# Performance work log

Hardware: AMD Instinct MI355X
Metric: run time of the kernel (lower is better)

## Reference

```python
import jax, jax.numpy as jnp
import numpy as np

N_NODES = 100000
N_EDGES = 1600000
IN_FEATS = 256
HIDDEN = 128
N_CLASSES = 128
NEG_SLOPE = 0.2


def setup_inputs() -> dict:
    key = jax.random.key(0)
    ks = jax.random.split(key, 12)
    inp = {
        "features": jax.random.normal(ks[0], (N_NODES, IN_FEATS), dtype=jnp.float32),
        "src": jax.random.randint(ks[1], (N_EDGES,), 0, N_NODES, dtype=jnp.int32),
        "dst": jax.random.randint(ks[2], (N_EDGES,), 0, N_NODES, dtype=jnp.int32),
        # layer 1 params (Xavier-ish scale)
        "W1": jax.random.normal(ks[3], (HIDDEN, IN_FEATS), dtype=jnp.float32) / np.sqrt(IN_FEATS),
        "al1": jax.random.normal(ks[4], (HIDDEN,), dtype=jnp.float32) / np.sqrt(HIDDEN),
        "ar1": jax.random.normal(ks[5], (HIDDEN,), dtype=jnp.float32) / np.sqrt(HIDDEN),
        "b1": jnp.zeros((HIDDEN,), dtype=jnp.float32),
        # layer 2 params
        "W2": jax.random.normal(ks[6], (N_CLASSES, HIDDEN), dtype=jnp.float32) / np.sqrt(HIDDEN),
        "al2": jax.random.normal(ks[7], (N_CLASSES,), dtype=jnp.float32) / np.sqrt(N_CLASSES),
        "ar2": jax.random.normal(ks[8], (N_CLASSES,), dtype=jnp.float32) / np.sqrt(N_CLASSES),
        "b2": jnp.zeros((N_CLASSES,), dtype=jnp.float32),
    }
    return inp


def _gat_conv(x, W, attn_l, attn_r, bias, src, dst):
    """Single-head DGL GATConv: fc -> edge leaky-relu scores -> segment softmax over dst -> scatter-sum."""
    h = x @ W.T                                   # [N, D]
    el = h @ attn_l                               # [N]
    er = h @ attn_r                               # [N]
    e = jax.nn.leaky_relu(el[src] + er[dst], NEG_SLOPE)   # [E]
    # numerically stable segment softmax over incoming edges of each dst node
    m = jax.ops.segment_max(e, dst, num_segments=N_NODES)          # [N] (-inf for empty)
    ex = jnp.exp(e - m[dst])                                       # [E]
    s = jax.ops.segment_sum(ex, dst, num_segments=N_NODES)         # [N]
    alpha = ex / s[dst]                                            # [E]
    out = jax.ops.segment_sum(h[src] * alpha[:, None], dst, num_segments=N_NODES)
    return out + bias


def reference(features, src, dst, W1, al1, ar1, b1, W2, al2, ar2, b2):
    x = _gat_conv(features, W1, al1, ar1, b1, src, dst)
    x = jax.nn.elu(x)
    return _gat_conv(x, W2, al2, ar2, b2, src, dst)
```

## Files before the change

### kernel.cpp

```cpp
#include <hip/hip_runtime.h>

typedef unsigned short u16;
typedef unsigned int u32;

#define NEG_SLOPE 0.2f
#define BSHIFT 8
#define MAXBUCK 1024

using short8 = __attribute__((ext_vector_type(8))) short;
using float4v = __attribute__((ext_vector_type(4))) float;

__device__ __forceinline__ float bfu(u16 v) { return __uint_as_float(((u32)v) << 16); }
__device__ __forceinline__ float bflo(u32 u) { return __uint_as_float(u << 16); }
__device__ __forceinline__ float bfhi(u32 u) { return __uint_as_float(u & 0xffff0000u); }
__device__ __forceinline__ u16 f2bf(float f) {
  u32 x = __float_as_uint(f);
  return (u16)((x + 0x7fffu + ((x >> 16) & 1u)) >> 16);
}
__device__ __forceinline__ float loadf(const void* p, int idx, int isbf) {
  return isbf ? bfu(((const u16*)p)[idx]) : ((const float*)p)[idx];
}

__global__ __launch_bounds__(256) void detect_dtype(const u32* __restrict__ w,
                                                    int nwords, int* __restrict__ flag) {
  __shared__ int cnt;
  if (threadIdx.x == 0) cnt = 0;
  __syncthreads();
  int c = 0;
  for (int i = threadIdx.x; i < nwords; i += 256) {
    u32 e = (w[i] >> 7) & 0xFFu;
    c += (e >= 0x60u && e <= 0x90u) ? 1 : 0;
  }
  atomicAdd(&cnt, c);
  __syncthreads();
  if (threadIdx.x == 0) flag[0] = (cnt * 2 > nwords) ? 1 : 0;
}

__global__ __launch_bounds__(256) void scanA(int* __restrict__ a,
                                             int* __restrict__ bsum, int M) {
  __shared__ int sh[256];
  int t = threadIdx.x;
  int idx = blockIdx.x * 256 + t;
  int v = (idx < M) ? a[idx] : 0;
  sh[t] = v;
  __syncthreads();
  for (int off = 1; off < 256; off <<= 1) {
    int y = (t >= off) ? sh[t - off] : 0;
    __syncthreads();
    sh[t] += y;
    __syncthreads();
  }
  if (idx < M) a[idx] = sh[t] - v;
  if (t == 255) bsum[blockIdx.x] = sh[255];
}

__global__ __launch_bounds__(512) void scanBseq(int* __restrict__ a, int MB) {
  __shared__ int sh[512];
  __shared__ int carry;
  int t = threadIdx.x;
  if (t == 0) carry = 0;
  __syncthreads();
  for (int base = 0; base < MB; base += 512) {
    int v = (base + t < MB) ? a[base + t] : 0;
    sh[t] = v;
    __syncthreads();
    for (int off = 1; off < 512; off <<= 1) {
      int y = (t >= off) ? sh[t - off] : 0;
      __syncthreads();
      sh[t] += y;
      __syncthreads();
    }
    int c0 = carry;
    int excl = sh[t] - v + c0;
    int tot = sh[511];
    __syncthreads();
    if (t == 0) carry = c0 + tot;
    if (base + t < MB) a[base + t] = excl;
    __syncthreads();
  }
}

__global__ __launch_bounds__(256) void scanC(int* __restrict__ a,
                                             const int* __restrict__ boff, int M) {
  int idx = blockIdx.x * 256 + threadIdx.x;
  if (idx < M) a[idx] += boff[blockIdx.x];
}

__global__ __launch_bounds__(256) void part_scatter(const int* __restrict__ src,
                                                    const int* __restrict__ dst,
                                                    const int* __restrict__ Gh,
                                                    int* __restrict__ pd,
                                                    int* __restrict__ ps,
                                                    int E, int PB, int nbuck) {
  __shared__ int cur[MAXBUCK];
  int t = threadIdx.x;
  int blk = blockIdx.x;
  for (int i = t; i < nbuck; i += 256) cur[i] = Gh[(size_t)i * PB + blk];
  __syncthreads();
  int pbase = blk * 4096;
#pragma unroll
  for (int j = 0; j < 16; ++j) {
    int e = pbase + j * 256 + t;
    if (e < E) {
      int d = dst[e];
      int s = src[e];
      u32 b = (u32)d >> BSHIFT;
      if (b < (u32)nbuck) {
        int slot = atomicAdd(&cur[b], 1);
        if ((u32)slot < (u32)E) {
          pd[slot] = d;
          ps[slot] = s;
        }
      }
    }
  }
}

__global__ __launch_bounds__(256) void bucket_sort(const int* __restrict__ pd,
                                                   const int* __restrict__ ps,
                                                   const int* __restrict__ Gh,
                                                   int* __restrict__ indptr,
                                                   int* __restrict__ ssrc,
                                                   int E, int N, int PB, int nbuck) {
  __shared__ int bins[256];
  __shared__ int sh[256];
  __shared__ int cur[256];
  int t = threadIdx.x;
  int b = blockIdx.x;
  int base = Gh[(size_t)b * PB];
  int nextb = (b + 1 < nbuck) ? Gh[(size_t)(b + 1) * PB] : E;
  int sz = nextb - base;

  bins[t] = 0;
  __syncthreads();
  for (int i = t; i < sz; i += 256) atomicAdd(&bins[pd[base + i] & 255], 1);
  __syncthreads();

  int v = bins[t];
  sh[t] = v;
  __syncthreads();
  for (int off = 1; off < 256; off <<= 1) {
    int y = (t >= off) ? sh[t - off] : 0;
    __syncthreads();
    sh[t] += y;
    __syncthreads();
  }
  int excl = sh[t] - v;
  int node = b * 256 + t;
  if (node < N) indptr[node] = base + excl;
  if (b == 0 && t == 0) indptr[N] = E;
  cur[t] = excl;
  __syncthreads();

  for (int i = t; i < sz; i += 256) {
    int d = pd[base + i];
    int slot = atomicAdd(&cur[d & 255], 1);
    u32 gidx = (u32)(base + slot);
    if (gidx < (u32)E) ssrc[gidx] = ps[base + i];
  }
}

__global__ __launch_bounds__(256) void bsw_build(const void* __restrict__ W,
                                                 u16* __restrict__ Bsw, int K,
                                                 const int* __restrict__ dflag) {
  const int isbf = dflag[0];
  int t = blockIdx.x * 256 + threadIdx.x;
  int total = (K / 32) * 8 * 64;
  if (t >= total) return;
  int lane = t & 63;
  int c = (t >> 6) & 7;
  int ktile = t >> 9;
  int n = lane & 15, q = lane >> 4;
  int col = c * 16 + n;
  u16 vals[8];
#pragma unroll
  for (int j = 0; j < 8; ++j) {
    int k = ktile * 32 + q * 8 + j;
    int idx = col * K + k;
    vals[j] = isbf ? ((const u16*)W)[idx] : f2bf(((const float*)W)[idx]);
  }
  *(uint4*)(Bsw + (size_t)t * 8) = *(uint4*)vals;
}

template <int K, int ISBF>
__device__ __forceinline__ void gemm_core(const void* __restrict__ Xv,
                                          const u16* __restrict__ Bsw,
                                          const int* mclamp, int q, int lane,
                                          float4v acc[2][8]) {
  constexpr int NT = K / 32;
  const uint4* btb = (const uint4*)Bsw + lane;
  if (ISBF) {
    const u16* X0 = (const u16*)Xv + (size_t)mclamp[0] * K + q * 8;
    const u16* X1 = (const u16*)Xv + (size_t)mclamp[1] * K + q * 8;
    short8 a0 = *(const short8*)X0;
    short8 a1 = *(const short8*)X1;
#pragma unroll
    for (int t = 0; t < NT; ++t) {
      short8 n0 = a0, n1 = a1;
      if (t + 1 < NT) {
        n0 = *(const short8*)(X0 + (t + 1) * 32);
        n1 = *(const short8*)(X1 + (t + 1) * 32);
      }
      const uint4* bt = btb + (size_t)t * 8 * 64;
#pragma unroll
      for (int c = 0; c < 8; ++c) {
        uint4 bw = bt[c * 64];
        short8 bf = *(short8*)&bw;
        acc[0][c] = __builtin_amdgcn_mfma_f32_16x16x32_bf16(a0, bf, acc[0][c], 0, 0, 0);
        acc[1][c] = __builtin_amdgcn_mfma_f32_16x16x32_bf16(a1, bf, acc[1][c], 0, 0, 0);
      }
      a0 = n0;
      a1 = n1;
    }
  } else {
    const float* X0 = (const float*)Xv + (size_t)mclamp[0] * K + q * 8;
    const float* X1 = (const float*)Xv + (size_t)mclamp[1] * K + q * 8;
    float4 f00 = *(const float4*)X0, f01 = *(const float4*)(X0 + 4);
    float4 f10 = *(const float4*)X1, f11 = *(const float4*)(X1 + 4);
#pragma unroll
    for (int t = 0; t < NT; ++t) {
      float4 g00 = f00, g01 = f01, g10 = f10, g11 = f11;
      if (t + 1 < NT) {
        g00 = *(const float4*)(X0 + (t + 1) * 32);
        g01 = *(const float4*)(X0 + (t + 1) * 32 + 4);
        g10 = *(const float4*)(X1 + (t + 1) * 32);
        g11 = *(const float4*)(X1 + (t + 1) * 32 + 4);
      }
      u16 t0[8] = {f2bf(f00.x), f2bf(f00.y), f2bf(f00.z), f2bf(f00.w),
                   f2bf(f01.x), f2bf(f01.y), f2bf(f01.z), f2bf(f01.w)};
      u16 t1[8] = {f2bf(f10.x), f2bf(f10.y), f2bf(f10.z), f2bf(f10.w),
                   f2bf(f11.x), f2bf(f11.y), f2bf(f11.z), f2bf(f11.w)};
      short8 a0 = *(short8*)t0;
      short8 a1 = *(short8*)t1;
      const uint4* bt = btb + (size_t)t * 8 * 64;
#pragma unroll
      for (int c = 0; c < 8; ++c) {
        uint4 bw = bt[c * 64];
        short8 bf = *(short8*)&bw;
        acc[0][c] = __builtin_amdgcn_mfma_f32_16x16x32_bf16(a0, bf, acc[0][c], 0, 0, 0);
        acc[1][c] = __builtin_amdgcn_mfma_f32_16x16x32_bf16(a1, bf, acc[1][c], 0, 0, 0);
      }
      f00 = g00; f01 = g01; f10 = g10; f11 = g11;
    }
  }
}

template <int K, int DYNA>
__device__ __forceinline__ void gemm_body(int bix, const void* __restrict__ Xv,
                                          const u16* __restrict__ Bsw,
                                          u16* __restrict__ Hb,
                                          const void* __restrict__ al,
                                          const void* __restrict__ ar,
                                          float* __restrict__ el_,
                                          float* __restrict__ er_, int N,
                                          const int* __restrict__ dflag) {
  const int isbfP = dflag[0];
  int tid = threadIdx.x;
  int w = tid >> 6, lane = tid & 63;
  int n = lane & 15, q = lane >> 4;
  int base = bix * 128 + w * 32;

  int mclamp[2];
#pragma unroll
  for (int mt = 0; mt < 2; ++mt) {
    int m = base + mt * 16 + n;
    mclamp[mt] = (m < N) ? m : 0;
  }

  float alv[8], arv[8];
#pragma unroll
  for (int c = 0; c < 8; ++c) {
    alv[c] = loadf(al, c * 16 + n, isbfP);
    arv[c] = loadf(ar, c * 16 + n, isbfP);
  }

  float4v acc[2][8];
#pragma unroll
  for (int mt = 0; mt < 2; ++mt)
#pragma unroll
    for (int c = 0; c < 8; ++c) acc[mt][c] = (float4v){0.f, 0.f, 0.f, 0.f};

  if (DYNA == 0 || isbfP) {
    gemm_core<K, 1>(Xv, Bsw, mclamp, q, lane, acc);
  } else {
    gemm_core<K, 0>(Xv, Bsw, mclamp, q, lane, acc);
  }

#pragma unroll
  for (int mt = 0; mt < 2; ++mt)
#pragma unroll
    for (int c = 0; c < 8; ++c) {
#pragma unroll
      for (int r = 0; r < 4; ++r) {
        int row = base + mt * 16 + q * 4 + r;
        if (row < N) Hb[(size_t)row * 128 + c * 16 + n] = f2bf(acc[mt][c][r]);
      }
    }

#pragma unroll
  for (int mt = 0; mt < 2; ++mt)
#pragma unroll
    for (int r = 0; r < 4; ++r) {
      float sl = 0.f, sr = 0.f;
#pragma unroll
      for (int c = 0; c < 8; ++c) {
        float v = acc[mt][c][r];
        sl = fmaf(v, alv[c], sl);
        sr = fmaf(v, arv[c], sr);
      }
#pragma unroll
      for (int off = 1; off < 16; off <<= 1) {
        sl += __shfl_xor(sl, off);
        sr += __shfl_xor(sr, off);
      }
      if (n == 0) {
        int row = base + mt * 16 + q * 4 + r;
        if (row < N) {
          el_[row] = sl;
          er_[row] = sr;
        }
      }
    }
}

template <int K, int DYNA>
__global__ __launch_bounds__(256) void gemm_mfma(const void* __restrict__ Xv,
                                                 const u16* __restrict__ Bsw,
                                                 u16* __restrict__ Hb,
                                                 const void* __restrict__ al,
                                                 const void* __restrict__ ar,
                                                 float* __restrict__ el_,
                                                 float* __restrict__ er_, int N,
                                                 const int* __restrict__ dflag) {
  gemm_body<K, DYNA>(blockIdx.x, Xv, Bsw, Hb, al, ar, el_, er_, N, dflag);
}

template <int K, int DYNA>
__global__ __launch_bounds__(256) void fused_gemm_hist(
    const void* __restrict__ Xv, const u16* __restrict__ Bsw, u16* __restrict__ Hb,
    const void* __restrict__ al, const void* __restrict__ ar,
    float* __restrict__ el_, float* __restrict__ er_, int N,
    const int* __restrict__ dflag, int gemm_blocks,
    const int* __restrict__ dst, int* __restrict__ Gh, int E, int PB, int nbuck) {
  __shared__ int hcnt[MAXBUCK];
  int bix = (int)blockIdx.x;
  if (bix < gemm_blocks) {
    gemm_body<K, DYNA>(bix, Xv, Bsw, Hb, al, ar, el_, er_, N, dflag);
    return;
  }
  int pblk = bix - gemm_blocks;
  int t = threadIdx.x;
  for (int i = t; i < nbuck; i += 256) hcnt[i] = 0;
  __syncthreads();
  int pbase = pblk * 4096;
#pragma unroll
  for (int j = 0; j < 16; ++j) {
    int e = pbase + j * 256 + t;
    if (e < E) {
      u32 b = (u32)dst[e] >> BSHIFT;
      if (b < (u32)nbuck) atomicAdd(&hcnt[b], 1);
    }
  }
  __syncthreads();
  for (int i = t; i < nbuck; i += 256) Gh[(size_t)i * PB + pblk] = hcnt[i];
}

template <int MODE>
__global__ __launch_bounds__(256) void agg_kernel(const u32* __restrict__ Hb,
                                                  const float* __restrict__ el,
                                                  const float* __restrict__ er,
                                                  const int* __restrict__ indptr,
                                                  const int* __restrict__ ssrc,
                                                  const void* __restrict__ bias,
                                                  void* __restrict__ outv, int N,
                                                  const int* __restrict__ dflag) {
  const int isbf = dflag[0];
  int tid = threadIdx.x;
  int n = blockIdx.x * 4 + (tid >> 6);
  int lane = tid & 63;
  if (n >= N) return;

  int beg = indptr[n];
  int end = indptr[n + 1];
  float ern = er[n];

  float aa0 = 0.f, aa1 = 0.f;
  float m_run = -INFINITY, l_run = 0.f;

  for (int p = beg; p < end; p += 64) {
    int rem = end - p;
    int valid = lane < rem;
    int ide = valid ? ssrc[p + lane] : 0;

    float sc = el[ide] + ern;
    sc = (sc > 0.f) ? sc : NEG_SLOPE * sc;
    sc = valid ? sc : -INFINITY;

    float mc = sc;
#pragma unroll
    for (int off = 1; off < 64; off <<= 1) mc = fmaxf(mc, __shfl_xor(mc, off));

    float m_new = fmaxf(m_run, mc);
    float corr = __expf(m_run - m_new);
    float pe = __expf(sc - m_new);

    float ls = pe;
#pragma unroll
    for (int off = 1; off < 64; off <<= 1) ls += __shfl_xor(ls, off);

    l_run = l_run * corr + ls;
    aa0 *= corr;
    aa1 *= corr;
    m_run = m_new;

    int cl = (rem < 64) ? rem : 64;
    int e = 0;
    for (; e + 8 <= cl; e += 8) {
      int id_[8];
      u32 h_[8];
#pragma unroll
      for (int k = 0; k < 8; ++k) id_[k] = __builtin_amdgcn_readlane(ide, e + k);
#pragma unroll
      for (int k = 0; k < 8; ++k) h_[k] = Hb[(size_t)id_[k] * 64 + lane];
#pragma unroll
      for (int k = 0; k < 8; ++k) {
        float pk = __int_as_float(__builtin_amdgcn_readlane(__float_as_int(pe), e + k));
        aa0 = fmaf(pk, bflo(h_[k]), aa0);
        aa1 = fmaf(pk, bfhi(h_[k]), aa1);
      }
    }
    for (; e + 4 <= cl; e += 4) {
      int id_[4];
      u32 h_[4];
#pragma unroll
      for (int k = 0; k < 4; ++k) id_[k] = __builtin_amdgcn_readlane(ide, e + k);
#pragma unroll
      for (int k = 0; k < 4; ++k) h_[k] = Hb[(size_t)id_[k] * 64 + lane];
#pragma unroll
      for (int k = 0; k < 4; ++k) {
        float pk = __int_as_float(__builtin_amdgcn_readlane(__float_as_int(pe), e + k));
        aa0 = fmaf(pk, bflo(h_[k]), aa0);
        aa1 = fmaf(pk, bfhi(h_[k]), aa1);
      }
    }
    for (; e < cl; ++e) {
      int i0 = __builtin_amdgcn_readlane(ide, e);
      u32 h0 = Hb[(size_t)i0 * 64 + lane];
      float p0 = __int_as_float(__builtin_amdgcn_readlane(__float_as_int(pe), e));
      aa0 = fmaf(p0, bflo(h0), aa0);
      aa1 = fmaf(p0, bfhi(h0), aa1);
    }
  }

  float inv = (l_run > 0.f) ? 1.f / l_run : 0.f;
  float o0 = aa0 * inv + loadf(bias, 2 * lane, isbf);
  float o1 = aa1 * inv + loadf(bias, 2 * lane + 1, isbf);

  if (MODE == 0) {
    o0 = (o0 > 0.f) ? o0 : (__expf(o0) - 1.f);
    o1 = (o1 > 0.f) ? o1 : (__expf(o1) - 1.f);
    ((u32*)outv)[(size_t)n * 64 + lane] = (u32)f2bf(o0) | ((u32)f2bf(o1) << 16);
  } else {
    if (isbf) {
      ((u32*)outv)[(size_t)n * 64 + lane] = (u32)f2bf(o0) | ((u32)f2bf(o1) << 16);
    } else {
      ((float2*)outv)[(size_t)n * 64 + lane] = make_float2(o0, o1);
    }
  }
}


extern "C" void kernel_launch(void* const* d_in, const int* in_sizes, int n_in,
                              void* d_out, int out_size, void* d_ws, size_t ws_size,
                              hipStream_t stream) {
  const int IN_FEATS = 256, HID = 128;
  const void* features = d_in[0];
  const int* src = (const int*)d_in[1];
  const int* dst = (const int*)d_in[2];
  const void* W1 = d_in[3];
  const void* al1 = d_in[4];
  const void* ar1 = d_in[5];
  const void* b1 = d_in[6];
  const void* W2 = d_in[7];
  const void* al2 = d_in[8];
  const void* ar2 = d_in[9];
  const void* b2 = d_in[10];

  const int N = in_sizes[0] / IN_FEATS;
  const int E = in_sizes[1];

  char* p = (char*)d_ws;
  auto alloc = [&](size_t bytes) -> void* {
    void* q = (void*)p;
    p += (bytes + 255) & ~(size_t)255;
    return q;
  };
  int* dflag = (int*)alloc(256);
  u16* Bsw1 = (u16*)alloc((size_t)(IN_FEATS / 32) * 8 * 64 * 8 * 2);
  u16* Bsw2 = (u16*)alloc((size_t)(HID / 32) * 8 * 64 * 8 * 2);
  u16* hb = (u16*)alloc((size_t)N * HID * 2);
  u16* x = (u16*)alloc((size_t)N * HID * 2);
  float* el = (float*)alloc((size_t)N * 4);
  float* er = (float*)alloc((size_t)N * 4);
  int* indptr = (int*)alloc((size_t)(N + 1) * 4);

  const int nbuck = (N + 255) >> BSHIFT;
  const int PB = (E + 4095) / 4096;
  const int M = nbuck * PB;
  const int MB1 = (M + 255) / 256;

  int* Gh = (int*)alloc((size_t)M * 4);
  int* bsumA = (int*)alloc((size_t)MB1 * 4);
  int* ssrc = (int*)alloc((size_t)E * 4);

  int* pd = (int*)x;
  int* ps = (int*)((char*)x + (((size_t)E * 4 + 255) & ~(size_t)255));

  const int GEMM_B = (N + 127) / 128;
  const int NODE_B = (N + 3) / 4;

  detect_dtype<<<1, 256, 0, stream>>>((const u32*)features, 4096, dflag);
  bsw_build<<<((IN_FEATS / 32) * 8 * 64 + 255) / 256, 256, 0, stream>>>(W1, Bsw1, IN_FEATS, dflag);
  bsw_build<<<((HID / 32) * 8 * 64 + 255) / 256, 256, 0, stream>>>(W2, Bsw2, HID, dflag);

  fused_gemm_hist<IN_FEATS, 1><<<GEMM_B + PB, 256, 0, stream>>>(
      features, Bsw1, hb, al1, ar1, el, er, N, dflag, GEMM_B, dst, Gh, E, PB, nbuck);

  scanA<<<MB1, 256, 0, stream>>>(Gh, bsumA, M);
  scanBseq<<<1, 512, 0, stream>>>(bsumA, MB1);
  scanC<<<MB1, 256, 0, stream>>>(Gh, bsumA, M);

  part_scatter<<<PB, 256, 0, stream>>>(src, dst, Gh, pd, ps, E, PB, nbuck);
  bucket_sort<<<nbuck, 256, 0, stream>>>(pd, ps, Gh, indptr, ssrc, E, N, PB, nbuck);

  agg_kernel<0><<<NODE_B, 256, 0, stream>>>((const u32*)hb, el, er, indptr, ssrc, b1, (void*)x, N, dflag);

  gemm_mfma<HID, 0><<<GEMM_B, 256, 0, stream>>>((const void*)x, Bsw2, hb, al2, ar2, el, er, N, dflag);
  agg_kernel<1><<<NODE_B, 256, 0, stream>>>((const u32*)hb, el, er, indptr, ssrc, b2, d_out, N, dflag);
}
```

Baseline: 468.7 us.

## Fold scan offsets into consumers, stage GEMM weights in LDS, specialize low-degree aggregation

```diff
diff --git a/kernel.cpp b/kernel.cpp
--- a/kernel.cpp
+++ b/kernel.cpp
@@ -9,6 +9,7 @@
 
 using short8 = __attribute__((ext_vector_type(8))) short;
 using float4v = __attribute__((ext_vector_type(4))) float;
+using float2v = __attribute__((ext_vector_type(2))) float;
 
 __device__ __forceinline__ float bfu(u16 v) { return __uint_as_float(((u32)v) << 16); }
 __device__ __forceinline__ float bflo(u32 u) { return __uint_as_float(u << 16); }
@@ -80,22 +81,20 @@
   }
 }
 
-__global__ __launch_bounds__(256) void scanC(int* __restrict__ a,
-                                             const int* __restrict__ boff, int M) {
-  int idx = blockIdx.x * 256 + threadIdx.x;
-  if (idx < M) a[idx] += boff[blockIdx.x];
-}
-
 __global__ __launch_bounds__(256) void part_scatter(const int* __restrict__ src,
                                                     const int* __restrict__ dst,
                                                     const int* __restrict__ Gh,
+                                                    const int* __restrict__ bsumA,
                                                     int* __restrict__ pd,
                                                     int* __restrict__ ps,
                                                     int E, int PB, int nbuck) {
   __shared__ int cur[MAXBUCK];
   int t = threadIdx.x;
   int blk = blockIdx.x;
-  for (int i = t; i < nbuck; i += 256) cur[i] = Gh[(size_t)i * PB + blk];
+  for (int i = t; i < nbuck; i += 256) {
+    int j = i * PB + blk;
+    cur[i] = Gh[j] + bsumA[j >> 8];
+  }
   __syncthreads();
   int pbase = blk * 4096;
 #pragma unroll
@@ -119,6 +118,7 @@
 __global__ __launch_bounds__(256) void bucket_sort(const int* __restrict__ pd,
                                                    const int* __restrict__ ps,
                                                    const int* __restrict__ Gh,
+                                                   const int* __restrict__ bsumA,
                                                    int* __restrict__ indptr,
                                                    int* __restrict__ ssrc,
                                                    int E, int N, int PB, int nbuck) {
@@ -127,8 +127,13 @@
   __shared__ int cur[256];
   int t = threadIdx.x;
   int b = blockIdx.x;
-  int base = Gh[(size_t)b * PB];
-  int nextb = (b + 1 < nbuck) ? Gh[(size_t)(b + 1) * PB] : E;
+  int j0 = b * PB;
+  int base = Gh[j0] + bsumA[j0 >> 8];
+  int nextb = E;
+  if (b + 1 < nbuck) {
+    int j1 = (b + 1) * PB;
+    nextb = Gh[j1] + bsumA[j1 >> 8];
+  }
   int sz = nextb - base;
 
   bins[t] = 0;
@@ -182,13 +187,26 @@
   *(uint4*)(Bsw + (size_t)t * 8) = *(uint4*)vals;
 }
 
+template <int K>
+__device__ __forceinline__ void stage_bsw(const u16* __restrict__ Bsw, u16* Bs, int tid) {
+  constexpr int PASSES = (K * 256) / 4096;
+  int w = tid >> 6, lane = tid & 63;
+#pragma unroll
+  for (int i = 0; i < PASSES; ++i) {
+    int off = i * 4096 + w * 1024;
+    __builtin_amdgcn_global_load_lds(
+        (const __attribute__((address_space(1))) u32*)((const char*)Bsw + off + lane * 16),
+        (__attribute__((address_space(3))) u32*)((char*)Bs + off), 16, 0, 0);
+  }
+}
+
 template <int K, int ISBF>
 __device__ __forceinline__ void gemm_core(const void* __restrict__ Xv,
-                                          const u16* __restrict__ Bsw,
+                                          const u16* Bs,
                                           const int* mclamp, int q, int lane,
                                           float4v acc[2][8]) {
   constexpr int NT = K / 32;
-  const uint4* btb = (const uint4*)Bsw + lane;
+  const uint4* btb = (const uint4*)Bs + lane;
   if (ISBF) {
     const u16* X0 = (const u16*)Xv + (size_t)mclamp[0] * K + q * 8;
     const u16* X1 = (const u16*)Xv + (size_t)mclamp[1] * K + q * 8;
@@ -254,12 +272,15 @@
                                           float* __restrict__ el_,
                                           float* __restrict__ er_, int N,
                                           const int* __restrict__ dflag) {
+  __shared__ __align__(16) u16 Bs[(K / 32) * 8 * 64 * 8];
   const int isbfP = dflag[0];
   int tid = threadIdx.x;
   int w = tid >> 6, lane = tid & 63;
   int n = lane & 15, q = lane >> 4;
   int base = bix * 128 + w * 32;
 
+  stage_bsw<K>(Bsw, Bs, tid);
+
   int mclamp[2];
 #pragma unroll
   for (int mt = 0; mt < 2; ++mt) {
@@ -280,10 +301,12 @@
 #pragma unroll
     for (int c = 0; c < 8; ++c) acc[mt][c] = (float4v){0.f, 0.f, 0.f, 0.f};
 
+  __syncthreads();
+
   if (DYNA == 0 || isbfP) {
-    gemm_core<K, 1>(Xv, Bsw, mclamp, q, lane, acc);
+    gemm_core<K, 1>(Xv, Bs, mclamp, q, lane, acc);
   } else {
-    gemm_core<K, 0>(Xv, Bsw, mclamp, q, lane, acc);
+    gemm_core<K, 0>(Xv, Bs, mclamp, q, lane, acc);
   }
 
 #pragma unroll
@@ -382,40 +405,29 @@
 
   int beg = indptr[n];
   int end = indptr[n + 1];
+  int deg = end - beg;
   float ern = er[n];
 
-  float aa0 = 0.f, aa1 = 0.f;
-  float m_run = -INFINITY, l_run = 0.f;
-
-  for (int p = beg; p < end; p += 64) {
-    int rem = end - p;
-    int valid = lane < rem;
-    int ide = valid ? ssrc[p + lane] : 0;
-
+  float2v acc = {0.f, 0.f};
+  float inv;
+
+  if (deg <= 64) {
+    int valid = lane < deg;
+    int ide = valid ? ssrc[beg + lane] : 0;
     float sc = el[ide] + ern;
     sc = (sc > 0.f) ? sc : NEG_SLOPE * sc;
     sc = valid ? sc : -INFINITY;
 
-    float mc = sc;
-#pragma unroll
-    for (int off = 1; off < 64; off <<= 1) mc = fmaxf(mc, __shfl_xor(mc, off));
-
-    float m_new = fmaxf(m_run, mc);
-    float corr = __expf(m_run - m_new);
-    float pe = __expf(sc - m_new);
-
-    float ls = pe;
-#pragma unroll
-    for (int off = 1; off < 64; off <<= 1) ls += __shfl_xor(ls, off);
-
-    l_run = l_run * corr + ls;
-    aa0 *= corr;
-    aa1 *= corr;
-    m_run = m_new;
-
-    int cl = (rem < 64) ? rem : 64;
+    float m = sc;
+#pragma unroll
+    for (int off = 1; off < 64; off <<= 1) m = fmaxf(m, __shfl_xor(m, off));
+    float pe = __expf(sc - m);
+    float l = pe;
+#pragma unroll
+    for (int off = 1; off < 64; off <<= 1) l += __shfl_xor(l, off);
+
     int e = 0;
-    for (; e + 8 <= cl; e += 8) {
+    for (; e + 8 <= deg; e += 8) {
       int id_[8];
       u32 h_[8];
 #pragma unroll
@@ -425,11 +437,12 @@
 #pragma unroll
       for (int k = 0; k < 8; ++k) {
         float pk = __int_as_float(__builtin_amdgcn_readlane(__float_as_int(pe), e + k));
-        aa0 = fmaf(pk, bflo(h_[k]), aa0);
-        aa1 = fmaf(pk, bfhi(h_[k]), aa1);
-      }
-    }
-    for (; e + 4 <= cl; e += 4) {
+        float2v hv = {bflo(h_[k]), bfhi(h_[k])};
+        float2v pv = {pk, pk};
+        acc = pv * hv + acc;
+      }
+    }
+    for (; e + 4 <= deg; e += 4) {
       int id_[4];
       u32 h_[4];
 #pragma unroll
@@ -439,22 +452,74 @@
 #pragma unroll
       for (int k = 0; k < 4; ++k) {
         float pk = __int_as_float(__builtin_amdgcn_readlane(__float_as_int(pe), e + k));
-        aa0 = fmaf(pk, bflo(h_[k]), aa0);
-        aa1 = fmaf(pk, bfhi(h_[k]), aa1);
-      }
-    }
-    for (; e < cl; ++e) {
+        float2v hv = {bflo(h_[k]), bfhi(h_[k])};
+        float2v pv = {pk, pk};
+        acc = pv * hv + acc;
+      }
+    }
+    for (; e < deg; ++e) {
       int i0 = __builtin_amdgcn_readlane(ide, e);
       u32 h0 = Hb[(size_t)i0 * 64 + lane];
-      float p0 = __int_as_float(__builtin_amdgcn_readlane(__float_as_int(pe), e));
-      aa0 = fmaf(p0, bflo(h0), aa0);
-      aa1 = fmaf(p0, bfhi(h0), aa1);
-    }
-  }
-
-  float inv = (l_run > 0.f) ? 1.f / l_run : 0.f;
-  float o0 = aa0 * inv + loadf(bias, 2 * lane, isbf);
-  float o1 = aa1 * inv + loadf(bias, 2 * lane + 1, isbf);
+      float pk = __int_as_float(__builtin_amdgcn_readlane(__float_as_int(pe), e));
+      float2v hv = {bflo(h0), bfhi(h0)};
+      float2v pv = {pk, pk};
+      acc = pv * hv + acc;
+    }
+    inv = (deg > 0 && l > 0.f) ? 1.f / l : 0.f;
+  } else {
+    float m_run = -INFINITY, l_run = 0.f;
+    for (int p = beg; p < end; p += 64) {
+      int rem = end - p;
+      int valid = lane < rem;
+      int ide = valid ? ssrc[p + lane] : 0;
+      float sc = el[ide] + ern;
+      sc = (sc > 0.f) ? sc : NEG_SLOPE * sc;
+      sc = valid ? sc : -INFINITY;
+      float mc = sc;
+#pragma unroll
+      for (int off = 1; off < 64; off <<= 1) mc = fmaxf(mc, __shfl_xor(mc, off));
+      float m_new = fmaxf(m_run, mc);
+      float corr = __expf(m_run - m_new);
+      float pe = __expf(sc - m_new);
+      float ls = pe;
+#pragma unroll
+      for (int off = 1; off < 64; off <<= 1) ls += __shfl_xor(ls, off);
+      l_run = l_run * corr + ls;
+      float2v cv = {corr, corr};
+      acc = acc * cv;
+      m_run = m_new;
+
+      int cl = (rem < 64) ? rem : 64;
+      int e = 0;
+      for (; e + 8 <= cl; e += 8) {
+        int id_[8];
+        u32 h_[8];
+#pragma unroll
+        for (int k = 0; k < 8; ++k) id_[k] = __builtin_amdgcn_readlane(ide, e + k);
+#pragma unroll
+        for (int k = 0; k < 8; ++k) h_[k] = Hb[(size_t)id_[k] * 64 + lane];
+#pragma unroll
+        for (int k = 0; k < 8; ++k) {
+          float pk = __int_as_float(__builtin_amdgcn_readlane(__float_as_int(pe), e + k));
+          float2v hv = {bflo(h_[k]), bfhi(h_[k])};
+          float2v pv = {pk, pk};
+          acc = pv * hv + acc;
+        }
+      }
+      for (; e < cl; ++e) {
+        int i0 = __builtin_amdgcn_readlane(ide, e);
+        u32 h0 = Hb[(size_t)i0 * 64 + lane];
+        float pk = __int_as_float(__builtin_amdgcn_readlane(__float_as_int(pe), e));
+        float2v hv = {bflo(h0), bfhi(h0)};
+        float2v pv = {pk, pk};
+        acc = pv * hv + acc;
+      }
+    }
+    inv = (l_run > 0.f) ? 1.f / l_run : 0.f;
+  }
+
+  float o0 = acc.x * inv + loadf(bias, 2 * lane, isbf);
+  float o1 = acc.y * inv + loadf(bias, 2 * lane + 1, isbf);
 
   if (MODE == 0) {
     o0 = (o0 > 0.f) ? o0 : (__expf(o0) - 1.f);
@@ -528,10 +593,9 @@
 
   scanA<<<MB1, 256, 0, stream>>>(Gh, bsumA, M);
   scanBseq<<<1, 512, 0, stream>>>(bsumA, MB1);
-  scanC<<<MB1, 256, 0, stream>>>(Gh, bsumA, M);
-
-  part_scatter<<<PB, 256, 0, stream>>>(src, dst, Gh, pd, ps, E, PB, nbuck);
-  bucket_sort<<<nbuck, 256, 0, stream>>>(pd, ps, Gh, indptr, ssrc, E, N, PB, nbuck);
+
+  part_scatter<<<PB, 256, 0, stream>>>(src, dst, Gh, bsumA, pd, ps, E, PB, nbuck);
+  bucket_sort<<<nbuck, 256, 0, stream>>>(pd, ps, Gh, bsumA, indptr, ssrc, E, N, PB, nbuck);
 
   agg_kernel<0><<<NODE_B, 256, 0, stream>>>((const u32*)hb, el, er, indptr, ssrc, b1, (void*)x, N, dflag);
 
```

Result: faster. 452.9 us (-3.4%).
